# Kernel optimization log

Measured on AMD Instinct MI355X. Metric: run time of the kernel, lower is better.

## Reference

```python
import jax, jax.numpy as jnp
import numpy as np
import math

NUM_HEADS = 16
D_MODEL = 1024
D_HEAD = D_MODEL // NUM_HEADS
B, S = 2, 2048


def setup_inputs() -> dict:
    key = jax.random.key(0)
    k1, k2 = jax.random.split(key)
    query = jax.random.normal(k1, (B, S, D_MODEL), dtype=jnp.float32)
    # causal mask: True where masked (j > i)
    mask = jnp.broadcast_to(jnp.triu(jnp.ones((S, S), dtype=bool), k=1), (B, S, S))
    W_o = jax.random.normal(k2, (D_MODEL, D_MODEL), dtype=jnp.float32) * (1.0 / math.sqrt(D_MODEL))
    b_o = jnp.zeros((D_MODEL,), dtype=jnp.float32)
    return {"query": query, "mask": mask, "W_o": W_o, "b_o": b_o}


def reference(query, mask, W_o, b_o):
    # NOTE: faithful to source — q/k/v linear layers are never applied in forward.
    # Self-attention: key = value = query.
    Bq, Sq, D = query.shape
    # split heads: [B, S, D] -> [B, H, S, dh]
    q = query.reshape(Bq, Sq, NUM_HEADS, D_HEAD).transpose(0, 2, 1, 3)
    k = q
    v = q
    # logits: [B, H, Sq, Sk]
    logits = jnp.einsum("bhqd,bhkd->bhqk", q, k) / math.sqrt(D_HEAD)
    logits = jnp.where(mask[:, None, :, :], -jnp.inf, logits)
    attn = jax.nn.softmax(logits, axis=-1)          # [B, H, Sq, Sk]
    out = jnp.einsum("bhqk,bhkd->bhqd", attn, v)    # [B, H, Sq, dh]
    # merge heads: [B, Sq, D]
    out = out.transpose(0, 2, 1, 3).reshape(Bq, Sq, D)
    # output projection (torch Linear: x @ W.T + b)
    return out @ W_o.T + b_o
```

## Files before the change

kernel.cpp:

```cpp
#include <hip/hip_runtime.h>
#include <hip/hip_bf16.h>
#include <stdint.h>

#define SEQ 2048
#define DMODEL 1024

typedef __attribute__((ext_vector_type(8))) short short8;
typedef __attribute__((ext_vector_type(4))) short short4v;
typedef __attribute__((ext_vector_type(4))) float floatx4;

__device__ __forceinline__ floatx4 mfma16x16x32(short8 a, short8 b, floatx4 c) {
  return __builtin_amdgcn_mfma_f32_16x16x32_bf16(a, b, c, 0, 0, 0);
}

__device__ __forceinline__ floatx4 mfma16x16x16(short4v a, short4v b, floatx4 c) {
  return __builtin_amdgcn_mfma_f32_16x16x16bf16_1k(a, b, c, 0, 0, 0);
}

__device__ __forceinline__ uint16_t f2bf(float x) {
  __hip_bfloat16 h = __float2bfloat16(x);
  return *reinterpret_cast<uint16_t*>(&h);
}

__device__ __forceinline__ float bf2f(uint16_t u) {
  uint32_t x = (uint32_t)u << 16;
  union { uint32_t u; float f; } c; c.u = x; return c.f;
}

__device__ __forceinline__ void glds16(const uint16_t* g, uint16_t* l) {
  __builtin_amdgcn_global_load_lds(
      (const __attribute__((address_space(1))) uint32_t*)g,
      (__attribute__((address_space(3))) uint32_t*)(uint32_t)(uintptr_t)l,
      16, 0, 0);
}

__global__ __launch_bounds__(256) void cvt_kernel(
    const float* __restrict__ q, uint16_t* __restrict__ qd,
    const float* __restrict__ w, uint16_t* __restrict__ wd,
    int nq4, int ntot4) {
  int i = blockIdx.x * 256 + threadIdx.x;
  if (i >= ntot4) return;
  const float* src = (i < nq4) ? q : w;
  uint16_t* dst = (i < nq4) ? qd : wd;
  int j = (i < nq4) ? i : i - nq4;
  float4 v = ((const float4*)src)[j];
  ushort4 r;
  r.x = f2bf(v.x); r.y = f2bf(v.y); r.z = f2bf(v.z); r.w = f2bf(v.w);
  ((ushort4*)dst)[j] = r;
}

__device__ __forceinline__ int vt_idx(int d, int key) {
  return d * 64 + ((((key >> 3) ^ (d >> 3) ^ d) & 7) << 3) + (key & 7);
}

__global__ __launch_bounds__(256, 2) void attn_kernel(
    const uint16_t* __restrict__ qbf, uint16_t* __restrict__ Opart,
    float* __restrict__ Lpart) {
  const int w    = blockIdx.x >> 5;
  const int qt   = 15 - (w >> 1);
  const int half = w & 1;
  const int bh   = blockIdx.x & 31;
  const int b    = bh >> 4;
  const int h    = bh & 15;
  const int tid  = threadIdx.x;
  const int wave = tid >> 6;
  const int lane = tid & 63;
  const int l15  = lane & 15;
  const int quad = lane >> 4;

  __shared__ uint16_t Kt[2][64 * 64];
  __shared__ uint16_t Vt[2][64 * 64];

  const uint16_t* base = qbf + (size_t)b * SEQ * DMODEL + h * 64;

  short8 qf[2][2];
  #pragma unroll
  for (int s = 0; s < 2; ++s)
    #pragma unroll
    for (int ks = 0; ks < 2; ++ks)
      qf[s][ks] = *(const short8*)(base +
          (size_t)(qt * 128 + s * 64 + wave * 16 + l15) * DMODEL + ks * 32 + quad * 8);

  floatx4 o_acc[2][4];
  float l_run[2];
  #pragma unroll
  for (int s = 0; s < 2; ++s) {
    #pragma unroll
    for (int dt = 0; dt < 4; ++dt) o_acc[s][dt] = (floatx4){0.f, 0.f, 0.f, 0.f};
    l_run[s] = 0.f;
  }

  const int r0 = tid >> 3;
  const int cg = (tid & 7) * 8;
  const int krow = tid >> 3;
  const int kcg  = tid & 7;

  auto stage = [&](int kt, int buf) {
    #pragma unroll
    for (int rr = 0; rr < 2; ++rr) {
      int row = rr * 32 + krow;
      glds16(base + (size_t)(kt * 64 + row) * DMODEL + ((kcg ^ (row & 7)) * 8),
             &Kt[buf][row * 64 + kcg * 8]);
    }
    uint4 v0 = *(const uint4*)(base + (size_t)(kt * 64 + 2 * r0) * DMODEL + cg);
    uint4 v1 = *(const uint4*)(base + (size_t)(kt * 64 + 2 * r0 + 1) * DMODEL + cg);
    uint16_t t0[8], t1[8];
    *(uint4*)t0 = v0;
    *(uint4*)t1 = v1;
    #pragma unroll
    for (int i = 0; i < 8; ++i) {
      uint32_t pk = (uint32_t)t0[i] | ((uint32_t)t1[i] << 16);
      *(uint32_t*)&Vt[buf][vt_idx(cg + i, 2 * r0)] = pk;
    }
  };

  const int ktlo = half ? (qt + 1) : 0;
  const int kthi = half ? (2 * qt + 1) : qt;
  stage(ktlo, ktlo & 1);

  auto iter = [&](int kt, int nt0, int nt1, bool d0, bool d1) {
    __syncthreads();
    if (kt < kthi) stage(kt + 1, (kt + 1) & 1);
    const int buf = kt & 1;

    floatx4 sacc[2][4];
    #pragma unroll
    for (int s = 0; s < 2; ++s)
      #pragma unroll
      for (int nt = 0; nt < 4; ++nt) sacc[s][nt] = (floatx4){0.f, 0.f, 0.f, 0.f};

    #pragma unroll
    for (int ks = 0; ks < 2; ++ks)
      #pragma unroll
      for (int nt = 0; nt < 4; ++nt) {
        if (nt > nt0 && nt > nt1) continue;
        int row = nt * 16 + l15;
        short8 kf = *(const short8*)
            &Kt[buf][row * 64 + (((ks * 4 + quad) ^ (row & 7)) * 8)];
        if (nt <= nt0) sacc[0][nt] = mfma16x16x32(kf, qf[0][ks], sacc[0][nt]);
        if (nt <= nt1) sacc[1][nt] = mfma16x16x32(kf, qf[1][ks], sacc[1][nt]);
      }

    #pragma unroll
    for (int nt = 0; nt < 4; ++nt) {
      if (nt > nt0 && nt > nt1) continue;
      short4v vf[4];
      #pragma unroll
      for (int dt = 0; dt < 4; ++dt)
        vf[dt] = *(const short4v*)&Vt[buf][vt_idx(dt * 16 + l15, nt * 16 + quad * 4)];
      #pragma unroll
      for (int s = 0; s < 2; ++s) {
        const int ntm = s ? nt1 : nt0;
        const bool dg = s ? d1 : d0;
        if (nt > ntm) continue;
        short4v pf;
        #pragma unroll
        for (int r = 0; r < 4; ++r) {
          float p = __builtin_amdgcn_exp2f(fmaf(sacc[s][nt][r], 0.1803369f, -10.f));
          if (dg && nt == wave && quad * 4 + r > l15) p = 0.f;
          l_run[s] += p;
          pf[r] = (short)f2bf(p);
        }
        #pragma unroll
        for (int dt = 0; dt < 4; ++dt)
          o_acc[s][dt] = mfma16x16x16(pf, vf[dt], o_acc[s][dt]);
      }
    }
  };

  if (half == 0) {
    if (qt == 0) {
      iter(0, wave, 3, true, false);
    } else {
      for (int kt = 0; kt <= qt; ++kt) iter(kt, 3, 3, false, false);
    }
  } else {
    for (int kt = qt + 1; kt < 2 * qt; ++kt) iter(kt, 3, 3, false, false);
    if (qt >= 1) iter(2 * qt, wave, 3, true, false);
    iter(2 * qt + 1, -1, wave, false, true);
  }

  const size_t obase = (size_t)half * (4096 * 1024);
  #pragma unroll
  for (int s = 0; s < 2; ++s) {
    float l = l_run[s];
    l += __shfl_xor(l, 16, 64);
    l += __shfl_xor(l, 32, 64);
    int rowg = b * SEQ + qt * 128 + s * 64 + wave * 16 + l15;
    if (quad == 0) Lpart[half * 65536 + h * 4096 + rowg] = l;
    #pragma unroll
    for (int dt = 0; dt < 4; ++dt)
      #pragma unroll
      for (int r = 0; r < 4; ++r) {
        int rowo = b * SEQ + qt * 128 + s * 64 + wave * 16 + quad * 4 + r;
        Opart[obase + (size_t)rowo * DMODEL + h * 64 + dt * 16 + l15] =
            f2bf(o_acc[s][dt][r]);
      }
  }
}

__global__ __launch_bounds__(256) void combine_kernel(
    const uint16_t* __restrict__ Opart, const float* __restrict__ Lpart,
    uint16_t* __restrict__ X) {
  int i = blockIdx.x * 256 + threadIdx.x;
  int row = i >> 7;
  int c8  = (i & 127) * 8;
  int h   = c8 >> 6;
  float inv = 1.0f / (Lpart[h * 4096 + row] + Lpart[65536 + h * 4096 + row]);
  uint16_t a[8], bpt[8], o[8];
  *(uint4*)a   = *(const uint4*)&Opart[(size_t)row * DMODEL + c8];
  *(uint4*)bpt = *(const uint4*)&Opart[(size_t)4096 * 1024 + (size_t)row * DMODEL + c8];
  #pragma unroll
  for (int k = 0; k < 8; ++k)
    o[k] = f2bf((bf2f(a[k]) + bf2f(bpt[k])) * inv);
  *(uint4*)&X[(size_t)row * DMODEL + c8] = *(uint4*)o;
}

__global__ __launch_bounds__(256, 4) void proj_kernel(
    const uint16_t* __restrict__ X, const uint16_t* __restrict__ Wo,
    const float* __restrict__ bo, float* __restrict__ out) {
  const int bx = blockIdx.x;
  const int by = blockIdx.y;
  const int tid = threadIdx.x;
  const int wave = tid >> 6, lane = tid & 63, l15 = lane & 15, quad = lane >> 4;
  const int wr = wave >> 1, wc = wave & 1;

  __shared__ uint16_t As[2][128 * 64];
  __shared__ uint16_t Bs[2][64 * 64];

  floatx4 acc[4][2];
  #pragma unroll
  for (int mt = 0; mt < 4; ++mt)
    #pragma unroll
    for (int nt = 0; nt < 2; ++nt) acc[mt][nt] = (floatx4){0.f, 0.f, 0.f, 0.f};

  const int srow = tid >> 3;
  const int scg  = tid & 7;

  auto stage = [&](int kt, int buf) {
    #pragma unroll
    for (int rr = 0; rr < 4; ++rr) {
      int row = rr * 32 + srow;
      glds16(X + (size_t)(bx * 128 + row) * DMODEL + kt * 64 + ((scg ^ (row & 7)) * 8),
             &As[buf][row * 64 + scg * 8]);
    }
    #pragma unroll
    for (int rr = 0; rr < 2; ++rr) {
      int row = rr * 32 + srow;
      glds16(Wo + (size_t)(by * 64 + row) * DMODEL + kt * 64 + ((scg ^ (row & 7)) * 8),
             &Bs[buf][row * 64 + scg * 8]);
    }
  };

  stage(0, 0);
  for (int kt = 0; kt < 16; ++kt) {
    __syncthreads();
    if (kt < 15) stage(kt + 1, (kt + 1) & 1);
    const int buf = kt & 1;
    #pragma unroll
    for (int ks = 0; ks < 2; ++ks) {
      short8 af[4], bf2[2];
      #pragma unroll
      for (int mt = 0; mt < 4; ++mt) {
        int row = wr * 64 + mt * 16 + l15;
        af[mt] = *(const short8*)
            &As[buf][row * 64 + (((ks * 4 + quad) ^ (row & 7)) * 8)];
      }
      #pragma unroll
      for (int nt = 0; nt < 2; ++nt) {
        int row = wc * 32 + nt * 16 + l15;
        bf2[nt] = *(const short8*)
            &Bs[buf][row * 64 + (((ks * 4 + quad) ^ (row & 7)) * 8)];
      }
      #pragma unroll
      for (int mt = 0; mt < 4; ++mt)
        #pragma unroll
        for (int nt = 0; nt < 2; ++nt)
          acc[mt][nt] = mfma16x16x32(af[mt], bf2[nt], acc[mt][nt]);
    }
  }

  #pragma unroll
  for (int nt = 0; nt < 2; ++nt) {
    int colg = by * 64 + wc * 32 + nt * 16 + l15;
    float bias = bo[colg];
    #pragma unroll
    for (int mt = 0; mt < 4; ++mt)
      #pragma unroll
      for (int r2 = 0; r2 < 4; ++r2) {
        int rowg = bx * 128 + wr * 64 + mt * 16 + quad * 4 + r2;
        out[(size_t)rowg * DMODEL + colg] = acc[mt][nt][r2] + bias;
      }
  }
}

extern "C" void kernel_launch(void* const* d_in, const int* in_sizes, int n_in,
                              void* d_out, int out_size, void* d_ws, size_t ws_size,
                              hipStream_t stream) {
  const float* q_f32  = (const float*)d_in[0];
  const float* Wo_f32 = (const float*)d_in[2];
  const float* bo     = (const float*)d_in[3];
  float* out = (float*)d_out;

  uint16_t* qbf   = (uint16_t*)d_ws;
  uint16_t* X     = (uint16_t*)((char*)d_ws + (size_t)8 * 1024 * 1024);
  uint16_t* wobf  = (uint16_t*)((char*)d_ws + (size_t)16 * 1024 * 1024);
  uint16_t* Opart = (uint16_t*)((char*)d_ws + (size_t)18 * 1024 * 1024);
  float*    Lpart = (float*)((char*)d_ws + (size_t)34 * 1024 * 1024);

  const int nq4 = 2 * SEQ * DMODEL / 4;
  const int nw4 = DMODEL * DMODEL / 4;
  const int nt4 = nq4 + nw4;
  cvt_kernel<<<dim3((nt4 + 255) / 256), dim3(256), 0, stream>>>(
      q_f32, qbf, Wo_f32, wobf, nq4, nt4);

  attn_kernel<<<dim3(1024), dim3(256), 0, stream>>>(qbf, Opart, Lpart);
  combine_kernel<<<dim3(2048), dim3(256), 0, stream>>>(Opart, Lpart, X);
  proj_kernel<<<dim3(32, 16), dim3(256), 0, stream>>>(X, wobf, bo, out);
}
```

Measured before the change: 143.6 us.

## Split causal attention key range into variable number of parts per query tile

Replaces the fixed two-way key split per query tile with a split into 1 to 4 parts that grows with the tile's causal length, raising the grid from 1024 to 1280 blocks with more even per-block work. The combine kernel now sums a variable number of partial outputs and row sums, and the workspace layout moves Lpart to make room for four partial buffers. The aim is to cut the tail imbalance and improve occupancy in the attention kernel. The cost is more partial-output traffic and extra reads in the combine step.

```diff
diff --git a/kernel.cpp b/kernel.cpp
--- a/kernel.cpp
+++ b/kernel.cpp
@@ -56,10 +56,17 @@
 __global__ __launch_bounds__(256, 2) void attn_kernel(
     const uint16_t* __restrict__ qbf, uint16_t* __restrict__ Opart,
     float* __restrict__ Lpart) {
-  const int w    = blockIdx.x >> 5;
-  const int qt   = 15 - (w >> 1);
-  const int half = w & 1;
-  const int bh   = blockIdx.x & 31;
+  const int c  = 39 - (blockIdx.x >> 5);
+  const int bh = blockIdx.x & 31;
+  int qt, part, np;
+  if (c < 4)       { qt = c;                 part = 0;           np = 1; }
+  else if (c < 12) { qt = 4 + ((c - 4) >> 1); part = (c - 4) & 1; np = 2; }
+  else if (c < 24) { int d = c - 12; qt = 8 + d / 3;  part = d % 3;  np = 3; }
+  else             { int d = c - 24; qt = 12 + (d >> 2); part = d & 3; np = 4; }
+  const int nkt  = 2 * (qt + 1);
+  const int ktlo = part * nkt / np;
+  const int kthi = (part + 1) * nkt / np;
+
   const int b    = bh >> 4;
   const int h    = bh & 15;
   const int tid  = threadIdx.x;
@@ -114,13 +121,11 @@
     }
   };
 
-  const int ktlo = half ? (qt + 1) : 0;
-  const int kthi = half ? (2 * qt + 1) : qt;
   stage(ktlo, ktlo & 1);
 
   auto iter = [&](int kt, int nt0, int nt1, bool d0, bool d1) {
     __syncthreads();
-    if (kt < kthi) stage(kt + 1, (kt + 1) & 1);
+    if (kt + 1 < kthi) stage(kt + 1, (kt + 1) & 1);
     const int buf = kt & 1;
 
     floatx4 sacc[2][4];
@@ -168,26 +173,20 @@
     }
   };
 
-  if (half == 0) {
-    if (qt == 0) {
-      iter(0, wave, 3, true, false);
-    } else {
-      for (int kt = 0; kt <= qt; ++kt) iter(kt, 3, 3, false, false);
-    }
-  } else {
-    for (int kt = qt + 1; kt < 2 * qt; ++kt) iter(kt, 3, 3, false, false);
-    if (qt >= 1) iter(2 * qt, wave, 3, true, false);
-    iter(2 * qt + 1, -1, wave, false, true);
-  }
-
-  const size_t obase = (size_t)half * (4096 * 1024);
+  for (int kt = ktlo; kt < kthi; ++kt) {
+    if (kt < 2 * qt)       iter(kt, 3, 3, false, false);
+    else if (kt == 2 * qt) iter(kt, wave, 3, true, false);
+    else                   iter(kt, -1, wave, false, true);
+  }
+
+  const size_t obase = (size_t)part * (4096 * 1024);
   #pragma unroll
   for (int s = 0; s < 2; ++s) {
     float l = l_run[s];
     l += __shfl_xor(l, 16, 64);
     l += __shfl_xor(l, 32, 64);
     int rowg = b * SEQ + qt * 128 + s * 64 + wave * 16 + l15;
-    if (quad == 0) Lpart[half * 65536 + h * 4096 + rowg] = l;
+    if (quad == 0) Lpart[part * 65536 + h * 4096 + rowg] = l;
     #pragma unroll
     for (int dt = 0; dt < 4; ++dt)
       #pragma unroll
@@ -206,13 +205,24 @@
   int row = i >> 7;
   int c8  = (i & 127) * 8;
   int h   = c8 >> 6;
-  float inv = 1.0f / (Lpart[h * 4096 + row] + Lpart[65536 + h * 4096 + row]);
-  uint16_t a[8], bpt[8], o[8];
-  *(uint4*)a   = *(const uint4*)&Opart[(size_t)row * DMODEL + c8];
-  *(uint4*)bpt = *(const uint4*)&Opart[(size_t)4096 * 1024 + (size_t)row * DMODEL + c8];
-  #pragma unroll
-  for (int k = 0; k < 8; ++k)
-    o[k] = f2bf((bf2f(a[k]) + bf2f(bpt[k])) * inv);
+  int qt  = (row & 2047) >> 7;
+  int np  = (qt + 4) >> 2;
+  float lsum = 0.f;
+  float acc[8];
+  #pragma unroll
+  for (int k = 0; k < 8; ++k) acc[k] = 0.f;
+  for (int p = 0; p < np; ++p) {
+    lsum += Lpart[p * 65536 + h * 4096 + row];
+    uint16_t a[8];
+    *(uint4*)a = *(const uint4*)
+        &Opart[(size_t)p * 4096 * 1024 + (size_t)row * DMODEL + c8];
+    #pragma unroll
+    for (int k = 0; k < 8; ++k) acc[k] += bf2f(a[k]);
+  }
+  float inv = 1.0f / lsum;
+  uint16_t o[8];
+  #pragma unroll
+  for (int k = 0; k < 8; ++k) o[k] = f2bf(acc[k] * inv);
   *(uint4*)&X[(size_t)row * DMODEL + c8] = *(uint4*)o;
 }
 
@@ -306,7 +316,7 @@
   uint16_t* X     = (uint16_t*)((char*)d_ws + (size_t)8 * 1024 * 1024);
   uint16_t* wobf  = (uint16_t*)((char*)d_ws + (size_t)16 * 1024 * 1024);
   uint16_t* Opart = (uint16_t*)((char*)d_ws + (size_t)18 * 1024 * 1024);
-  float*    Lpart = (float*)((char*)d_ws + (size_t)34 * 1024 * 1024);
+  float*    Lpart = (float*)((char*)d_ws + (size_t)50 * 1024 * 1024);
 
   const int nq4 = 2 * SEQ * DMODEL / 4;
   const int nw4 = DMODEL * DMODEL / 4;
@@ -314,7 +324,7 @@
   cvt_kernel<<<dim3((nt4 + 255) / 256), dim3(256), 0, stream>>>(
       q_f32, qbf, Wo_f32, wobf, nq4, nt4);
 
-  attn_kernel<<<dim3(1024), dim3(256), 0, stream>>>(qbf, Opart, Lpart);
+  attn_kernel<<<dim3(1280), dim3(256), 0, stream>>>(qbf, Opart, Lpart);
   combine_kernel<<<dim3(2048), dim3(256), 0, stream>>>(Opart, Lpart, X);
   proj_kernel<<<dim3(32, 16), dim3(256), 0, stream>>>(X, wobf, bo, out);
 }
```

After: 150.9 us. +5.1%, slower.
